# Kernel optimization log

Hardware: AMD Instinct MI355X
Metric: run time of the kernel (lower is better)

## Reference

```python
import jax, jax.numpy as jnp
import numpy as np

K = 3; STRIDE = 1; PAD = 1; DIL = 1; KN = K * K * K  # num_pts = 27


def _trilinear_sample(vol, grid):
    """F.grid_sample 3D, mode=bilinear, padding=zeros, align_corners=False.
    vol: (C, D, H, W); grid: (od, oh, ow, 3) with xyz order in [-1, 1].
    Returns (C, od, oh, ow)."""
    C, D, H, W = vol.shape
    # unnormalize (align_corners=False)
    ix = ((grid[..., 0] + 1.0) * W - 1.0) * 0.5
    iy = ((grid[..., 1] + 1.0) * H - 1.0) * 0.5
    iz = ((grid[..., 2] + 1.0) * D - 1.0) * 0.5
    x0 = jnp.floor(ix); y0 = jnp.floor(iy); z0 = jnp.floor(iz)
    out = jnp.zeros((C,) + grid.shape[:-1], vol.dtype)
    for dz in (0, 1):
        for dy in (0, 1):
            for dx in (0, 1):
                xc = x0 + dx; yc = y0 + dy; zc = z0 + dz
                w = (1.0 - jnp.abs(ix - xc)) * (1.0 - jnp.abs(iy - yc)) * (1.0 - jnp.abs(iz - zc))
                valid = (xc >= 0) & (xc < W) & (yc >= 0) & (yc < H) & (zc >= 0) & (zc < D)
                xi = jnp.clip(xc, 0, W - 1).astype(jnp.int32)
                yi = jnp.clip(yc, 0, H - 1).astype(jnp.int32)
                zi = jnp.clip(zc, 0, D - 1).astype(jnp.int32)
                val = vol[:, zi, yi, xi]  # (C, od, oh, ow)
                out = out + val * (w * valid.astype(vol.dtype))[None]
    return out


def setup_inputs() -> dict:
    key = jax.random.key(0)
    k1, k2, k3 = jax.random.split(key, 3)
    N, C, D, H, W = 2, 64, 16, 32, 32
    inp = jax.random.normal(k1, (N, C, D, H, W), dtype=jnp.float32)
    offset = jax.random.normal(k2, (N, KN * 3, D, H, W), dtype=jnp.float32)
    weight = jax.random.normal(k3, (64, 64, KN), dtype=jnp.float32) * 0.05
    return {"input": inp, "offset": offset, "weight": weight}


def reference(input, offset, weight):
    N, C, D, H, W = input.shape
    od, oh, ow = offset.shape[2], offset.shape[3], offset.shape[4]
    f32 = input.dtype
    # base sampling mesh (align_corners=True style normalization, as original)
    z = (jnp.arange(od) * STRIDE - PAD + ((K - 1) // 2) * DIL).astype(f32)
    y = (jnp.arange(oh) * STRIDE - PAD + ((K - 1) // 2) * DIL).astype(f32)
    x = (jnp.arange(ow) * STRIDE - PAD + ((K - 1) // 2) * DIL).astype(f32)
    mz, my, mx = jnp.meshgrid(z, y, x, indexing="ij")
    norm = lambda v, S: (v - (S - 1) / 2.0) / ((S - 1) / 2.0)
    mesh = jnp.stack([norm(mx, W), norm(my, H), norm(mz, D)], axis=-1)  # (od,oh,ow,3)
    # offsets: channel layout per kernel point is (dz, dy, dx)
    off = offset.reshape(N, KN, 3, od, oh, ow)
    goff = jnp.stack([
        off[:, :, 2] / ((W - 1) / 2.0),
        off[:, :, 1] / ((H - 1) / 2.0),
        off[:, :, 0] / ((D - 1) / 2.0),
    ], axis=-1)  # (N, KN, od, oh, ow, 3) xyz
    grid = mesh[None, None] + goff
    # per-batch, per-kernel-point trilinear gather -> (N, KN, C, od, oh, ow)
    sampled = jax.vmap(lambda v, g: jax.vmap(lambda gg: _trilinear_sample(v, gg))(g))(input, grid)
    # grouped matmul: weight (O, C, KN) flattened C-major matches sampled layout
    out = jnp.einsum("ock,nkcdhw->nodhw", weight, sampled)
    return out
```

## Files before the change

### kernel.cpp

```cpp
#include <hip/hip_runtime.h>

typedef __attribute__((ext_vector_type(8))) short short8;
typedef __attribute__((ext_vector_type(4))) float floatx4;

constexpr int NB  = 2;
constexpr int CC  = 64;
constexpr int DD  = 16;
constexpr int HH  = 32;
constexpr int WW  = 32;
constexpr int KN_ = 27;
constexpr int OC  = 64;
constexpr int DHW = DD * HH * WW;
constexpr int TILE_P = 32;

__device__ __forceinline__ unsigned short f2bf(float f) {
    unsigned int u = __float_as_uint(f);
    return (unsigned short)((u + 0x7fffu + ((u >> 16) & 1u)) >> 16);
}

__global__ __launch_bounds__(256) void k_tin(const float* __restrict__ in,
                                             unsigned int* __restrict__ outu) {
    __shared__ float tile[64][65];
    int bid = blockIdx.x;
    int n   = bid >> 8;
    int v0  = (bid & 255) << 6;
    int t = threadIdx.x, lane = t & 63, row = t >> 6;
#pragma unroll
    for (int i = 0; i < 16; ++i) {
        int c = (i << 2) + row;
        tile[c][lane] = in[(size_t)(n * CC + c) * DHW + v0 + lane];
    }
    __syncthreads();
#pragma unroll
    for (int i = 0; i < 8; ++i) {
        int flat = i * 256 + t;
        int v = flat >> 5, cd = flat & 31;
        unsigned int lo = f2bf(tile[2 * cd][v]);
        unsigned int hi = f2bf(tile[2 * cd + 1][v]);
        outu[(size_t)(n * DHW + v0 + v) * 32 + cd] = lo | (hi << 16);
    }
}

__global__ __launch_bounds__(256) void k_wf(const float* __restrict__ w,
                                            unsigned short* __restrict__ wf) {
    int f = blockIdx.x * 256 + threadIdx.x;
    int i  = f & 7;
    int l  = (f >> 3) & 63;
    int wv = (f >> 9) & 3;
    int cc = (f >> 11) & 1;
    int k  = f >> 12;
    int o = wv * 16 + (l & 15);
    int c = cc * 32 + ((l >> 4) << 3) + i;
    wf[f] = f2bf(w[(o * CC + c) * KN_ + k]);
}

__global__ __launch_bounds__(256) void k_main(const unsigned short* __restrict__ inp,
                                              const unsigned short* __restrict__ wf,
                                              const float* __restrict__ offs,
                                              float* __restrict__ out) {
    __shared__ unsigned short S[2 * 32 * 64];

    int t   = threadIdx.x;
    int bid = blockIdx.x;
    int n   = bid >> 9;
    int p0  = (bid & 511) << 5;

    int sp = t >> 3;
    int cg = t & 7;
    int pa = p0 + sp;
    int dpos = pa >> 10, hpos = (pa >> 5) & 31, wpos = pa & 31;

    int wv = t >> 6, l = t & 63;
    int lrow = l & 15, lk = l >> 4;

    floatx4 acc0 = {0.f, 0.f, 0.f, 0.f};
    floatx4 acc1 = {0.f, 0.f, 0.f, 0.f};

    const float* offb = offs + (size_t)n * (3 * KN_) * DHW + pa;
    const unsigned short* inb = inp + ((size_t)n * DHW << 6);

    const int woff = sp * 64 + ((cg ^ (sp & 7)) << 3);
    const int prow1 = 16 + lrow;
    const int roff00 = lrow  * 64 + (((0 + lk) ^ (lrow  & 7)) << 3);
    const int roff10 = lrow  * 64 + (((4 + lk) ^ (lrow  & 7)) << 3);
    const int roff01 = prow1 * 64 + (((0 + lk) ^ (prow1 & 7)) << 3);
    const int roff11 = prow1 * 64 + (((4 + lk) ^ (prow1 & 7)) << 3);

    for (int k = 0; k < KN_; ++k) {
        const short8 wa0 = *(const short8*)(wf + (((k << 3) + 0 + wv) << 9) + (l << 3));
        const short8 wa1 = *(const short8*)(wf + (((k << 3) + 4 + wv) << 9) + (l << 3));

        float oz = offb[(k * 3 + 0) * DHW];
        float oy = offb[(k * 3 + 1) * DHW];
        float ox = offb[(k * 3 + 2) * DHW];
        float ix = ((float)wpos + ox) * (32.0f / 31.0f) - 0.5f;
        float iy = ((float)hpos + oy) * (32.0f / 31.0f) - 0.5f;
        float iz = ((float)dpos + oz) * (16.0f / 15.0f) - 0.5f;
        float xf = floorf(ix), yf = floorf(iy), zf = floorf(iz);
        float fx = ix - xf, fy = iy - yf, fz = iz - zf;
        int x0 = (int)xf, y0 = (int)yf, z0 = (int)zf;

        float wx0 = ((unsigned)x0       < (unsigned)WW) ? 1.f - fx : 0.f;
        float wx1 = ((unsigned)(x0 + 1) < (unsigned)WW) ? fx       : 0.f;
        float wy0 = ((unsigned)y0       < (unsigned)HH) ? 1.f - fy : 0.f;
        float wy1 = ((unsigned)(y0 + 1) < (unsigned)HH) ? fy       : 0.f;
        float wz0 = ((unsigned)z0       < (unsigned)DD) ? 1.f - fz : 0.f;
        float wz1 = ((unsigned)(z0 + 1) < (unsigned)DD) ? fz       : 0.f;

        int xc0 = min(max(x0, 0), WW - 1), xc1 = min(max(x0 + 1, 0), WW - 1);
        int yc0 = min(max(y0, 0), HH - 1), yc1 = min(max(y0 + 1, 0), HH - 1);
        int zc0 = min(max(z0, 0), DD - 1), zc1 = min(max(z0 + 1, 0), DD - 1);

        float wzy00 = wz0 * wy0, wzy01 = wz0 * wy1, wzy10 = wz1 * wy0, wzy11 = wz1 * wy1;
        int b00 = (zc0 * HH + yc0) * WW, b01 = (zc0 * HH + yc1) * WW;
        int b10 = (zc1 * HH + yc0) * WW, b11 = (zc1 * HH + yc1) * WW;

        const int vox[8] = {b00 + xc0, b00 + xc1, b01 + xc0, b01 + xc1,
                            b10 + xc0, b10 + xc1, b11 + xc0, b11 + xc1};
        const float cwt[8] = {wzy00 * wx0, wzy00 * wx1, wzy01 * wx0, wzy01 * wx1,
                              wzy10 * wx0, wzy10 * wx1, wzy11 * wx0, wzy11 * wx1};

        float s0 = 0.f, s1 = 0.f, s2 = 0.f, s3 = 0.f, s4 = 0.f, s5 = 0.f, s6 = 0.f, s7 = 0.f;
#pragma unroll
        for (int cr = 0; cr < 8; ++cr) {
            const uint4 v = *(const uint4*)(inb + ((size_t)vox[cr] << 6) + (cg << 3));
            float wgt = cwt[cr];
            s0 += wgt * __uint_as_float(v.x << 16);
            s1 += wgt * __uint_as_float(v.x & 0xffff0000u);
            s2 += wgt * __uint_as_float(v.y << 16);
            s3 += wgt * __uint_as_float(v.y & 0xffff0000u);
            s4 += wgt * __uint_as_float(v.z << 16);
            s5 += wgt * __uint_as_float(v.z & 0xffff0000u);
            s6 += wgt * __uint_as_float(v.w << 16);
            s7 += wgt * __uint_as_float(v.w & 0xffff0000u);
        }

        uint4 pk;
        pk.x = (unsigned int)f2bf(s0) | ((unsigned int)f2bf(s1) << 16);
        pk.y = (unsigned int)f2bf(s2) | ((unsigned int)f2bf(s3) << 16);
        pk.z = (unsigned int)f2bf(s4) | ((unsigned int)f2bf(s5) << 16);
        pk.w = (unsigned int)f2bf(s6) | ((unsigned int)f2bf(s7) << 16);
        *(uint4*)(S + ((k & 1) << 11) + woff) = pk;

        __syncthreads();

        const unsigned short* Sb = S + ((k & 1) << 11);
        const short8 bf00 = *(const short8*)(Sb + roff00);
        const short8 bf10 = *(const short8*)(Sb + roff10);
        const short8 bf01 = *(const short8*)(Sb + roff01);
        const short8 bf11 = *(const short8*)(Sb + roff11);
        acc0 = __builtin_amdgcn_mfma_f32_16x16x32_bf16(wa0, bf00, acc0, 0, 0, 0);
        acc0 = __builtin_amdgcn_mfma_f32_16x16x32_bf16(wa1, bf10, acc0, 0, 0, 0);
        acc1 = __builtin_amdgcn_mfma_f32_16x16x32_bf16(wa0, bf01, acc1, 0, 0, 0);
        acc1 = __builtin_amdgcn_mfma_f32_16x16x32_bf16(wa1, bf11, acc1, 0, 0, 0);
    }

    float* ob = out + ((size_t)n * OC + (wv << 4) + (lk << 2)) * DHW + p0 + lrow;
#pragma unroll
    for (int r = 0; r < 4; ++r) {
        ob[r * DHW]      = acc0[r];
        ob[r * DHW + 16] = acc1[r];
    }
}

__global__ __launch_bounds__(256) void k_fallback(const float* __restrict__ inp,
                                                  const float* __restrict__ wt,
                                                  const float* __restrict__ offs,
                                                  float* __restrict__ out) {
    __shared__ float Slds[64][68];
    __shared__ float Wlds[64 * 64];
    int bid = blockIdx.x;
    int n = bid >> 8;
    int p0 = (bid & 255) * 64;
    int t = threadIdx.x;
    int cq = t & 15, c0 = cq << 2, pslot = t >> 4;
    int ob = (t & 15) << 2, pb = (t >> 4) << 2;
    int swz_w = (((cq & 7) ^ (cq >> 3)) << 2);
    float acc[4][4] = {};
    const float* offbase = offs + (size_t)n * (KN_ * 3) * DHW;
    for (int k = 0; k < KN_; ++k) {
#pragma unroll
        for (int i = 0; i < 16; ++i) {
            int f = i * 256 + t;
            int o = f & 63, c = f >> 6;
            Wlds[f] = wt[(o * CC + c) * KN_ + k];
        }
#pragma unroll
        for (int j = 0; j < 4; ++j) {
            int pl = pslot + 16 * j;
            int pa = p0 + pl;
            int d = pa >> 10, h = (pa >> 5) & 31, w = pa & 31;
            float offz = offbase[(k * 3 + 0) * DHW + pa];
            float offy = offbase[(k * 3 + 1) * DHW + pa];
            float offx = offbase[(k * 3 + 2) * DHW + pa];
            float ix = ((float)w + offx) * (32.0f / 31.0f) - 0.5f;
            float iy = ((float)h + offy) * (32.0f / 31.0f) - 0.5f;
            float iz = ((float)d + offz) * (16.0f / 15.0f) - 0.5f;
            float xf = floorf(ix), yf = floorf(iy), zf = floorf(iz);
            float fx = ix - xf, fy = iy - yf, fz = iz - zf;
            int x0 = (int)xf, y0 = (int)yf, z0 = (int)zf;
            float wx0 = 1.0f - fx, wx1 = fx, wy0 = 1.0f - fy, wy1 = fy, wz0 = 1.0f - fz, wz1 = fz;
            float s0 = 0.f, s1 = 0.f, s2 = 0.f, s3 = 0.f;
#pragma unroll
            for (int dz = 0; dz < 2; ++dz) {
                int zc = z0 + dz;
                if ((unsigned)zc >= (unsigned)DD) continue;
                float wz = dz ? wz1 : wz0;
#pragma unroll
                for (int dy = 0; dy < 2; ++dy) {
                    int yc = y0 + dy;
                    if ((unsigned)yc >= (unsigned)HH) continue;
                    float wzy = wz * (dy ? wy1 : wy0);
#pragma unroll
                    for (int dx = 0; dx < 2; ++dx) {
                        int xc = x0 + dx;
                        if ((unsigned)xc >= (unsigned)WW) continue;
                        float wf = wzy * (dx ? wx1 : wx0);
                        int vox = (zc * HH + yc) * WW + xc;
                        const float* b = inp + (size_t)(n * CC + c0) * DHW + vox;
                        s0 += wf * b[0]; s1 += wf * b[DHW];
                        s2 += wf * b[2 * DHW]; s3 += wf * b[3 * DHW];
                    }
                }
            }
            int plw = pl ^ swz_w;
            Slds[c0 + 0][plw] = s0; Slds[c0 + 1][plw] = s1;
            Slds[c0 + 2][plw] = s2; Slds[c0 + 3][plw] = s3;
        }
        __syncthreads();
#pragma unroll
        for (int c = 0; c < 64; ++c) {
            const int g = ((c >> 2) & 7) ^ (c >> 5);
            float4 wv = *(const float4*)(Wlds + c * 64 + ob);
            float4 sv = *(const float4*)(&Slds[c][pb ^ (g << 2)]);
            float wa[4] = {wv.x, wv.y, wv.z, wv.w};
            float sa[4] = {sv.x, sv.y, sv.z, sv.w};
#pragma unroll
            for (int i = 0; i < 4; ++i)
#pragma unroll
                for (int jj = 0; jj < 4; ++jj) acc[i][jj] += wa[i] * sa[jj];
        }
        __syncthreads();
    }
#pragma unroll
    for (int i = 0; i < 4; ++i) {
        float4 vv;
        vv.x = acc[i][0]; vv.y = acc[i][1]; vv.z = acc[i][2]; vv.w = acc[i][3];
        *(float4*)(out + (size_t)(n * OC + ob + i) * DHW + p0 + pb) = vv;
    }
}

extern "C" void kernel_launch(void* const* d_in, const int* in_sizes, int n_in,
                              void* d_out, int out_size, void* d_ws, size_t ws_size,
                              hipStream_t stream) {
    const float* inp = (const float*)d_in[0];
    const float* off = (const float*)d_in[1];
    const float* wgt = (const float*)d_in[2];
    float* out = (float*)d_out;

    const size_t in_bf_bytes = (size_t)NB * DHW * CC * 2;
    const size_t wf_bytes    = (size_t)KN_ * 2 * 4 * 64 * 8 * 2;
    if (ws_size >= in_bf_bytes + wf_bytes) {
        unsigned int*   in_t = (unsigned int*)d_ws;
        unsigned short* w_f  = (unsigned short*)((char*)d_ws + in_bf_bytes);
        k_tin<<<dim3(NB * 256), dim3(256), 0, stream>>>(inp, in_t);
        k_wf<<<dim3((KN_ * CC * OC) / 256), dim3(256), 0, stream>>>(wgt, w_f);
        k_main<<<dim3(NB * 512), dim3(256), 0, stream>>>((const unsigned short*)in_t, w_f, off, out);
    } else {
        k_fallback<<<dim3(NB * 256), dim3(256), 0, stream>>>(inp, wgt, off, out);
    }
}
```

Before: 128.7 us.

## Switch gather and MFMA to fp16 with packed-half accumulation, merge prep kernels

Stores the transposed input and weights as fp16 instead of bf16 and does the trilinear blend with packed half8 multiply-adds, which removes the per-element unpack, fp32 accumulate and repack. The MFMA switches to the f16 variant, the two prep kernels are merged into one launch, and k_main gets a min-occupancy launch bound. Accumulating the interpolation in fp16 loses precision and risks overflow or tolerance failures compared with fp32 accumulation.

```diff
diff --git a/kernel.cpp b/kernel.cpp
--- a/kernel.cpp
+++ b/kernel.cpp
@@ -1,6 +1,7 @@
 #include <hip/hip_runtime.h>
 
 typedef __attribute__((ext_vector_type(8))) short short8;
+typedef __attribute__((ext_vector_type(8))) _Float16 half8;
 typedef __attribute__((ext_vector_type(4))) float floatx4;
 
 constexpr int NB  = 2;
@@ -11,53 +12,54 @@
 constexpr int KN_ = 27;
 constexpr int OC  = 64;
 constexpr int DHW = DD * HH * WW;
-constexpr int TILE_P = 32;
-
-__device__ __forceinline__ unsigned short f2bf(float f) {
-    unsigned int u = __float_as_uint(f);
-    return (unsigned short)((u + 0x7fffu + ((u >> 16) & 1u)) >> 16);
-}
-
-__global__ __launch_bounds__(256) void k_tin(const float* __restrict__ in,
-                                             unsigned int* __restrict__ outu) {
-    __shared__ float tile[64][65];
+
+__device__ __forceinline__ unsigned short f2h(float f) {
+    _Float16 h = (_Float16)f;
+    return *(unsigned short*)&h;
+}
+
+__global__ __launch_bounds__(256) void k_prep(const float* __restrict__ in,
+                                              const float* __restrict__ w,
+                                              unsigned int* __restrict__ outu,
+                                              unsigned short* __restrict__ wf) {
     int bid = blockIdx.x;
-    int n   = bid >> 8;
-    int v0  = (bid & 255) << 6;
-    int t = threadIdx.x, lane = t & 63, row = t >> 6;
-#pragma unroll
-    for (int i = 0; i < 16; ++i) {
-        int c = (i << 2) + row;
-        tile[c][lane] = in[(size_t)(n * CC + c) * DHW + v0 + lane];
-    }
-    __syncthreads();
-#pragma unroll
-    for (int i = 0; i < 8; ++i) {
-        int flat = i * 256 + t;
-        int v = flat >> 5, cd = flat & 31;
-        unsigned int lo = f2bf(tile[2 * cd][v]);
-        unsigned int hi = f2bf(tile[2 * cd + 1][v]);
-        outu[(size_t)(n * DHW + v0 + v) * 32 + cd] = lo | (hi << 16);
-    }
-}
-
-__global__ __launch_bounds__(256) void k_wf(const float* __restrict__ w,
-                                            unsigned short* __restrict__ wf) {
-    int f = blockIdx.x * 256 + threadIdx.x;
-    int i  = f & 7;
-    int l  = (f >> 3) & 63;
-    int wv = (f >> 9) & 3;
-    int cc = (f >> 11) & 1;
-    int k  = f >> 12;
-    int o = wv * 16 + (l & 15);
-    int c = cc * 32 + ((l >> 4) << 3) + i;
-    wf[f] = f2bf(w[(o * CC + c) * KN_ + k]);
-}
-
-__global__ __launch_bounds__(256) void k_main(const unsigned short* __restrict__ inp,
-                                              const unsigned short* __restrict__ wf,
-                                              const float* __restrict__ offs,
-                                              float* __restrict__ out) {
+    int t = threadIdx.x;
+    if (bid < 512) {
+        __shared__ float tile[64][65];
+        int n  = bid >> 8;
+        int v0 = (bid & 255) << 6;
+        int lane = t & 63, row = t >> 6;
+#pragma unroll
+        for (int i = 0; i < 16; ++i) {
+            int c = (i << 2) + row;
+            tile[c][lane] = in[(size_t)(n * CC + c) * DHW + v0 + lane];
+        }
+        __syncthreads();
+#pragma unroll
+        for (int i = 0; i < 8; ++i) {
+            int flat = i * 256 + t;
+            int v = flat >> 5, cd = flat & 31;
+            unsigned int lo = f2h(tile[2 * cd][v]);
+            unsigned int hi = f2h(tile[2 * cd + 1][v]);
+            outu[(size_t)(n * DHW + v0 + v) * 32 + cd] = lo | (hi << 16);
+        }
+    } else {
+        int f = (bid - 512) * 256 + t;
+        int i  = f & 7;
+        int l  = (f >> 3) & 63;
+        int wv = (f >> 9) & 3;
+        int cc = (f >> 11) & 1;
+        int k  = f >> 12;
+        int o = wv * 16 + (l & 15);
+        int c = cc * 32 + ((l >> 4) << 3) + i;
+        wf[f] = f2h(w[(o * CC + c) * KN_ + k]);
+    }
+}
+
+__global__ __launch_bounds__(256, 4) void k_main(const unsigned short* __restrict__ inp,
+                                                 const unsigned short* __restrict__ wf,
+                                                 const float* __restrict__ offs,
+                                                 float* __restrict__ out) {
     __shared__ unsigned short S[2 * 32 * 64];
 
     int t   = threadIdx.x;
@@ -87,8 +89,8 @@
     const int roff11 = prow1 * 64 + (((4 + lk) ^ (prow1 & 7)) << 3);
 
     for (int k = 0; k < KN_; ++k) {
-        const short8 wa0 = *(const short8*)(wf + (((k << 3) + 0 + wv) << 9) + (l << 3));
-        const short8 wa1 = *(const short8*)(wf + (((k << 3) + 4 + wv) << 9) + (l << 3));
+        const half8 wa0 = *(const half8*)(wf + (((k << 3) + 0 + wv) << 9) + (l << 3));
+        const half8 wa1 = *(const half8*)(wf + (((k << 3) + 4 + wv) << 9) + (l << 3));
 
         float oz = offb[(k * 3 + 0) * DHW];
         float oy = offb[(k * 3 + 1) * DHW];
@@ -120,39 +122,27 @@
         const float cwt[8] = {wzy00 * wx0, wzy00 * wx1, wzy01 * wx0, wzy01 * wx1,
                               wzy10 * wx0, wzy10 * wx1, wzy11 * wx0, wzy11 * wx1};
 
-        float s0 = 0.f, s1 = 0.f, s2 = 0.f, s3 = 0.f, s4 = 0.f, s5 = 0.f, s6 = 0.f, s7 = 0.f;
+        half8 acc = {0, 0, 0, 0, 0, 0, 0, 0};
 #pragma unroll
         for (int cr = 0; cr < 8; ++cr) {
-            const uint4 v = *(const uint4*)(inb + ((size_t)vox[cr] << 6) + (cg << 3));
-            float wgt = cwt[cr];
-            s0 += wgt * __uint_as_float(v.x << 16);
-            s1 += wgt * __uint_as_float(v.x & 0xffff0000u);
-            s2 += wgt * __uint_as_float(v.y << 16);
-            s3 += wgt * __uint_as_float(v.y & 0xffff0000u);
-            s4 += wgt * __uint_as_float(v.z << 16);
-            s5 += wgt * __uint_as_float(v.z & 0xffff0000u);
-            s6 += wgt * __uint_as_float(v.w << 16);
-            s7 += wgt * __uint_as_float(v.w & 0xffff0000u);
-        }
-
-        uint4 pk;
-        pk.x = (unsigned int)f2bf(s0) | ((unsigned int)f2bf(s1) << 16);
-        pk.y = (unsigned int)f2bf(s2) | ((unsigned int)f2bf(s3) << 16);
-        pk.z = (unsigned int)f2bf(s4) | ((unsigned int)f2bf(s5) << 16);
-        pk.w = (unsigned int)f2bf(s6) | ((unsigned int)f2bf(s7) << 16);
-        *(uint4*)(S + ((k & 1) << 11) + woff) = pk;
+            const half8 v = *(const half8*)(inb + ((size_t)vox[cr] << 6) + (cg << 3));
+            _Float16 wh = (_Float16)cwt[cr];
+            half8 w8 = {wh, wh, wh, wh, wh, wh, wh, wh};
+            acc += v * w8;
+        }
+        *(half8*)(S + ((k & 1) << 11) + woff) = acc;
 
         __syncthreads();
 
         const unsigned short* Sb = S + ((k & 1) << 11);
-        const short8 bf00 = *(const short8*)(Sb + roff00);
-        const short8 bf10 = *(const short8*)(Sb + roff10);
-        const short8 bf01 = *(const short8*)(Sb + roff01);
-        const short8 bf11 = *(const short8*)(Sb + roff11);
-        acc0 = __builtin_amdgcn_mfma_f32_16x16x32_bf16(wa0, bf00, acc0, 0, 0, 0);
-        acc0 = __builtin_amdgcn_mfma_f32_16x16x32_bf16(wa1, bf10, acc0, 0, 0, 0);
-        acc1 = __builtin_amdgcn_mfma_f32_16x16x32_bf16(wa0, bf01, acc1, 0, 0, 0);
-        acc1 = __builtin_amdgcn_mfma_f32_16x16x32_bf16(wa1, bf11, acc1, 0, 0, 0);
+        const half8 bf00 = *(const half8*)(Sb + roff00);
+        const half8 bf10 = *(const half8*)(Sb + roff10);
+        const half8 bf01 = *(const half8*)(Sb + roff01);
+        const half8 bf11 = *(const half8*)(Sb + roff11);
+        acc0 = __builtin_amdgcn_mfma_f32_16x16x32_f16(wa0, bf00, acc0, 0, 0, 0);
+        acc0 = __builtin_amdgcn_mfma_f32_16x16x32_f16(wa1, bf10, acc0, 0, 0, 0);
+        acc1 = __builtin_amdgcn_mfma_f32_16x16x32_f16(wa0, bf01, acc1, 0, 0, 0);
+        acc1 = __builtin_amdgcn_mfma_f32_16x16x32_f16(wa1, bf11, acc1, 0, 0, 0);
     }
 
     float* ob = out + ((size_t)n * OC + (wv << 4) + (lk << 2)) * DHW + p0 + lrow;
@@ -258,13 +248,12 @@
     const float* wgt = (const float*)d_in[2];
     float* out = (float*)d_out;
 
-    const size_t in_bf_bytes = (size_t)NB * DHW * CC * 2;
-    const size_t wf_bytes    = (size_t)KN_ * 2 * 4 * 64 * 8 * 2;
-    if (ws_size >= in_bf_bytes + wf_bytes) {
+    const size_t in_f16_bytes = (size_t)NB * DHW * CC * 2;
+    const size_t wf_bytes     = (size_t)KN_ * 2 * 4 * 64 * 8 * 2;
+    if (ws_size >= in_f16_bytes + wf_bytes) {
         unsigned int*   in_t = (unsigned int*)d_ws;
-        unsigned short* w_f  = (unsigned short*)((char*)d_ws + in_bf_bytes);
-        k_tin<<<dim3(NB * 256), dim3(256), 0, stream>>>(inp, in_t);
-        k_wf<<<dim3((KN_ * CC * OC) / 256), dim3(256), 0, stream>>>(wgt, w_f);
+        unsigned short* w_f  = (unsigned short*)((char*)d_ws + in_f16_bytes);
+        k_prep<<<dim3(512 + 432), dim3(256), 0, stream>>>(inp, wgt, in_t, w_f);
         k_main<<<dim3(NB * 512), dim3(256), 0, stream>>>((const unsigned short*)in_t, w_f, off, out);
     } else {
         k_fallback<<<dim3(NB * 256), dim3(256), 0, stream>>>(inp, wgt, off, out);
```

Measured after the change: 119.9 us. 1.07x faster.
